# Kernel optimization log

Measured on AMD Instinct MI355X. Metric: run time of the kernel, lower is better.

## Reference

```python
import jax, jax.numpy as jnp
import numpy as np

# AlphaFold2-scale config
C_S, C_Z, H, D = 256, 128, 8, 32
T = H * D  # total_dim = 256
B, S, N = 1, 128, 256  # batch, MSA rows, residues
EPS = 1e-5
SCALE = 1.0 / np.sqrt(D).astype(np.float32)


def _layer_norm(x, w, b):
    m = jnp.mean(x, axis=-1, keepdims=True)
    v = jnp.var(x, axis=-1, keepdims=True)
    return (x - m) * jax.lax.rsqrt(v + EPS) * w + b


def setup_inputs() -> dict:
    key = jax.random.key(0)
    ks = jax.random.split(key, 8)
    w = lambda k, shape: jax.random.normal(k, shape, dtype=jnp.float32) * 0.02
    return {
        "msa_representation": jax.random.normal(ks[0], (B, S, N, C_S), dtype=jnp.float32),
        "pair_representation": jax.random.normal(ks[1], (B, N, N, C_Z), dtype=jnp.float32),
        "ln_msa_w": jnp.ones((C_S,), jnp.float32),
        "ln_msa_b": jnp.zeros((C_S,), jnp.float32),
        "ln_pair_w": jnp.ones((C_Z,), jnp.float32),
        "ln_pair_b": jnp.zeros((C_Z,), jnp.float32),
        "Wq": w(ks[2], (C_S, T)),
        "Wk": w(ks[3], (C_S, T)),
        "Wv": w(ks[4], (C_S, T)),
        "Wpair": w(ks[5], (C_Z, H)),
        "Wg": w(ks[6], (C_S, T)),
        "bg": jnp.zeros((T,), jnp.float32),
        "Wo": w(ks[7], (T, C_S)),
        "bo": jnp.zeros((C_S,), jnp.float32),
    }


def reference(msa_representation, pair_representation, ln_msa_w, ln_msa_b,
              ln_pair_w, ln_pair_b, Wq, Wk, Wv, Wpair, Wg, bg, Wo, bo):
    msa = _layer_norm(msa_representation, ln_msa_w, ln_msa_b)  # [B,S,N,C_S]
    q = (msa @ Wq).reshape(B, S, N, H, D)
    k = (msa @ Wk).reshape(B, S, N, H, D)
    v = (msa @ Wv).reshape(B, S, N, H, D)
    g = jax.nn.sigmoid(msa @ Wg + bg).reshape(B, S, N, H, D)

    pair = _layer_norm(pair_representation, ln_pair_w, ln_pair_b)  # [B,N,N,C_Z]
    bias = jnp.transpose(pair @ Wpair, (0, 3, 1, 2))[:, None]  # [B,1,H,N,N]

    scores = jnp.einsum('bsihd,bsjhd->bshij', q, k) * SCALE + bias  # [B,S,H,N,N]
    attn = jax.nn.softmax(scores, axis=-1)
    vals = jnp.einsum('bshij,bsjhd->bsihd', attn, v)  # [B,S,N,H,D]
    vals = (g * vals).reshape(B, S, N, T)
    return vals @ Wo + bo  # [B,S,N,C_S]
```

## Files before the change

### kernel.cpp

```cpp
#include <hip/hip_runtime.h>

typedef unsigned short u16;
typedef unsigned int u32;
typedef __bf16 bf16x8 __attribute__((ext_vector_type(8)));
typedef float f32x4 __attribute__((ext_vector_type(4)));

#define EPS 1e-5f
#define SCALE 0.17677669529663687f

__device__ __forceinline__ u16 f2bf(float f) {
  u32 u = __builtin_bit_cast(u32, f);
  u32 r = (u + 0x7fffu + ((u >> 16) & 1u)) >> 16;
  return (u16)r;
}
__device__ __forceinline__ float bf2f(u16 v) {
  return __builtin_bit_cast(float, (u32)v << 16);
}

__device__ __forceinline__ void gload16(const u16* g, u16* l) {
  __builtin_amdgcn_global_load_lds(
      (const __attribute__((address_space(1))) void*)g,
      (__attribute__((address_space(3))) void*)l, 16, 0, 0);
}

__global__ __launch_bounds__(256) void k_ln_msa(const float* __restrict__ x,
                                                const float* __restrict__ w,
                                                const float* __restrict__ b,
                                                u16* __restrict__ y) {
  int wid = threadIdx.x >> 6, lane = threadIdx.x & 63;
  long row = (long)blockIdx.x * 4 + wid;
  const float4 v = *reinterpret_cast<const float4*>(x + row * 256 + lane * 4);
  float s = v.x + v.y + v.z + v.w;
  float ss = v.x * v.x + v.y * v.y + v.z * v.z + v.w * v.w;
#pragma unroll
  for (int off = 1; off < 64; off <<= 1) {
    s += __shfl_xor(s, off);
    ss += __shfl_xor(ss, off);
  }
  float m = s * (1.0f / 256.0f);
  float var = ss * (1.0f / 256.0f) - m * m;
  float rs = rsqrtf(var + EPS);
  int c = lane * 4;
  u16 o0 = f2bf((v.x - m) * rs * w[c + 0] + b[c + 0]);
  u16 o1 = f2bf((v.y - m) * rs * w[c + 1] + b[c + 1]);
  u16 o2 = f2bf((v.z - m) * rs * w[c + 2] + b[c + 2]);
  u16 o3 = f2bf((v.w - m) * rs * w[c + 3] + b[c + 3]);
  uint2 pk;
  pk.x = (u32)o0 | ((u32)o1 << 16);
  pk.y = (u32)o2 | ((u32)o3 << 16);
  *reinterpret_cast<uint2*>(y + row * 256 + c) = pk;
}

__global__ __launch_bounds__(256) void k_pair_bias(const float* __restrict__ x,
                                                   const float* __restrict__ w,
                                                   const float* __restrict__ b,
                                                   const float* __restrict__ Wp,
                                                   float* __restrict__ bias) {
  int wid = threadIdx.x >> 6, lane = threadIdx.x & 63;
  long row = (long)blockIdx.x * 4 + wid;
  const float2 v = *reinterpret_cast<const float2*>(x + row * 128 + lane * 2);
  float s = v.x + v.y, ss = v.x * v.x + v.y * v.y;
#pragma unroll
  for (int off = 1; off < 64; off <<= 1) {
    s += __shfl_xor(s, off);
    ss += __shfl_xor(ss, off);
  }
  float m = s * (1.0f / 128.0f);
  float var = ss * (1.0f / 128.0f) - m * m;
  float rs = rsqrtf(var + EPS);
  int c = lane * 2;
  float x0 = (v.x - m) * rs * w[c] + b[c];
  float x1 = (v.y - m) * rs * w[c + 1] + b[c + 1];
  const float4* wp = reinterpret_cast<const float4*>(Wp + (long)c * 8);
  float4 a0 = wp[0], a1 = wp[1], a2 = wp[2], a3 = wp[3];
  float p[8];
  p[0] = x0 * a0.x + x1 * a2.x; p[1] = x0 * a0.y + x1 * a2.y;
  p[2] = x0 * a0.z + x1 * a2.z; p[3] = x0 * a0.w + x1 * a2.w;
  p[4] = x0 * a1.x + x1 * a3.x; p[5] = x0 * a1.y + x1 * a3.y;
  p[6] = x0 * a1.z + x1 * a3.z; p[7] = x0 * a1.w + x1 * a3.w;
#pragma unroll
  for (int off = 1; off < 64; off <<= 1) {
#pragma unroll
    for (int h = 0; h < 8; h++) p[h] += __shfl_xor(p[h], off);
  }
  if (lane == 0) {
#pragma unroll
    for (int h = 0; h < 8; h++) bias[(long)h * 65536 + row] = p[h];
  }
}

__global__ __launch_bounds__(256) void k_prep_w(const float* __restrict__ Wq,
                                                const float* __restrict__ Wk,
                                                const float* __restrict__ Wv,
                                                const float* __restrict__ Wg,
                                                const float* __restrict__ Wo,
                                                u16* __restrict__ Wt,
                                                u16* __restrict__ WoT) {
  int tid = blockIdx.x * 256 + threadIdx.x;
  if (tid < 262144) {
    int n = tid >> 8, kk = tid & 255;
    int sel = n >> 8, c = n & 255;
    const float* W = (sel == 0) ? Wq : (sel == 1) ? Wk : (sel == 2) ? Wv : Wg;
    Wt[tid] = f2bf(W[kk * 256 + c]);
  } else {
    int t = tid - 262144;
    int n = t >> 8, kk = t & 255;
    WoT[t] = f2bf(Wo[kk * 256 + n]);
  }
}

__global__ __launch_bounds__(256) void k_proj(const u16* __restrict__ X,
                                              const u16* __restrict__ Wt,
                                              const float* __restrict__ bg,
                                              u16* __restrict__ P) {
  __shared__ u16 As[2][4096];
  __shared__ u16 Bs[2][4096];
  int tid = threadIdx.x;
  int wid = tid >> 6, lane = tid & 63;
  int lr = lane & 15, lg = lane >> 4;
  int wr = wid >> 1, wc = wid & 1;
  int m0 = blockIdx.x * 128;
  int n0 = blockIdx.y * 128;

  int tr = tid >> 2, tc = (tid & 3) * 8;
  const u16* gA0 = X + (long)(m0 + tr) * 256 + tc;
  const u16* gA1 = X + (long)(m0 + 64 + tr) * 256 + tc;
  const u16* gB0 = Wt + (long)(n0 + tr) * 256 + tc;
  const u16* gB1 = Wt + (long)(n0 + 64 + tr) * 256 + tc;

  f32x4 acc[4][4];
#pragma unroll
  for (int mi = 0; mi < 4; mi++)
#pragma unroll
    for (int ni = 0; ni < 4; ni++) acc[mi][ni] = (f32x4){0.f, 0.f, 0.f, 0.f};

#define STAGE(buf, k0)                                  \
  do {                                                  \
    gload16(gA0 + (k0), &As[buf][tid * 8]);             \
    gload16(gA1 + (k0), &As[buf][2048 + tid * 8]);      \
    gload16(gB0 + (k0), &Bs[buf][tid * 8]);             \
    gload16(gB1 + (k0), &Bs[buf][2048 + tid * 8]);      \
  } while (0)

  STAGE(0, 0);
  __syncthreads();
#pragma unroll
  for (int step = 0; step < 8; step++) {
    int buf = step & 1;
    if (step < 7) STAGE(buf ^ 1, (step + 1) * 32);
    bf16x8 a[4], b[4];
#pragma unroll
    for (int mi = 0; mi < 4; mi++)
      a[mi] = *reinterpret_cast<const bf16x8*>(&As[buf][(wr * 64 + mi * 16 + lr) * 32 + lg * 8]);
#pragma unroll
    for (int ni = 0; ni < 4; ni++)
      b[ni] = *reinterpret_cast<const bf16x8*>(&Bs[buf][(wc * 64 + ni * 16 + lr) * 32 + lg * 8]);
#pragma unroll
    for (int mi = 0; mi < 4; mi++)
#pragma unroll
      for (int ni = 0; ni < 4; ni++)
        acc[mi][ni] = __builtin_amdgcn_mfma_f32_16x16x32_bf16(a[mi], b[ni], acc[mi][ni], 0, 0, 0);
    __syncthreads();
  }
#undef STAGE

#pragma unroll
  for (int ni = 0; ni < 4; ni++) {
    int col = n0 + wc * 64 + ni * 16 + lr;
    bool isq = col < 256, isg = col >= 768;
    float bgv = isg ? bg[col - 768] : 0.f;
#pragma unroll
    for (int mi = 0; mi < 4; mi++) {
#pragma unroll
      for (int r = 0; r < 4; r++) {
        int row = m0 + wr * 64 + mi * 16 + lg * 4 + r;
        float val = acc[mi][ni][r];
        if (isq) val *= SCALE;
        else if (isg) val = 1.0f / (1.0f + __expf(-(val + bgv)));
        P[(long)row * 1024 + col] = f2bf(val);
      }
    }
  }
}

__global__ __launch_bounds__(256) void k_attn(const u16* __restrict__ P,
                                              const float* __restrict__ bias,
                                              u16* __restrict__ vals) {
  __shared__ alignas(16) u16 VT[32][264];
  __shared__ alignas(16) u16 Plds[4][16][264];
  int tid = threadIdx.x;
  int wid = tid >> 6, lane = tid & 63;
  int lr = lane & 15, lg = lane >> 4;
  int i0 = blockIdx.x * 64, h = blockIdx.y, s = blockIdx.z;
  long sbase = (long)s * 256;

  {
    int j = tid;
    const uint4* vp = reinterpret_cast<const uint4*>(P + (sbase + j) * 1024 + 512 + h * 32);
#pragma unroll
    for (int q4 = 0; q4 < 4; q4++) {
      uint4 u = vp[q4];
      VT[q4 * 8 + 0][j] = (u16)(u.x & 0xffff);
      VT[q4 * 8 + 1][j] = (u16)(u.x >> 16);
      VT[q4 * 8 + 2][j] = (u16)(u.y & 0xffff);
      VT[q4 * 8 + 3][j] = (u16)(u.y >> 16);
      VT[q4 * 8 + 4][j] = (u16)(u.z & 0xffff);
      VT[q4 * 8 + 5][j] = (u16)(u.z >> 16);
      VT[q4 * 8 + 6][j] = (u16)(u.w & 0xffff);
      VT[q4 * 8 + 7][j] = (u16)(u.w >> 16);
    }
  }
  __syncthreads();

  int iw0 = i0 + wid * 16;
  bf16x8 qa = *reinterpret_cast<const bf16x8*>(P + (sbase + iw0 + lr) * 1024 + h * 32 + lg * 8);
  f32x4 sc[16];
#pragma unroll
  for (int jt = 0; jt < 16; jt++) {
    bf16x8 kb = *reinterpret_cast<const bf16x8*>(
        P + (sbase + jt * 16 + lr) * 1024 + 256 + h * 32 + lg * 8);
    f32x4 z = (f32x4){0.f, 0.f, 0.f, 0.f};
    sc[jt] = __builtin_amdgcn_mfma_f32_16x16x32_bf16(qa, kb, z, 0, 0, 0);
  }

  const float* bp = bias + (long)h * 65536;
  float rmax[4] = {-1e30f, -1e30f, -1e30f, -1e30f};
#pragma unroll
  for (int jt = 0; jt < 16; jt++) {
#pragma unroll
    for (int r = 0; r < 4; r++) {
      float v = sc[jt][r] + bp[(iw0 + lg * 4 + r) * 256 + jt * 16 + lr];
      sc[jt][r] = v;
      rmax[r] = fmaxf(rmax[r], v);
    }
  }
#pragma unroll
  for (int off = 1; off < 16; off <<= 1) {
#pragma unroll
    for (int r = 0; r < 4; r++) rmax[r] = fmaxf(rmax[r], __shfl_xor(rmax[r], off));
  }
  float rsum[4] = {0.f, 0.f, 0.f, 0.f};
#pragma unroll
  for (int jt = 0; jt < 16; jt++) {
#pragma unroll
    for (int r = 0; r < 4; r++) {
      float pv = __expf(sc[jt][r] - rmax[r]);
      sc[jt][r] = pv;
      rsum[r] += pv;
    }
  }
#pragma unroll
  for (int off = 1; off < 16; off <<= 1) {
#pragma unroll
    for (int r = 0; r < 4; r++) rsum[r] += __shfl_xor(rsum[r], off);
  }
#pragma unroll
  for (int jt = 0; jt < 16; jt++) {
#pragma unroll
    for (int r = 0; r < 4; r++) Plds[wid][lg * 4 + r][jt * 16 + lr] = f2bf(sc[jt][r]);
  }

  f32x4 ao[2];
  ao[0] = (f32x4){0.f, 0.f, 0.f, 0.f};
  ao[1] = (f32x4){0.f, 0.f, 0.f, 0.f};
#pragma unroll
  for (int ks = 0; ks < 8; ks++) {
    bf16x8 pa = *reinterpret_cast<const bf16x8*>(&Plds[wid][lr][ks * 32 + lg * 8]);
#pragma unroll
    for (int nt = 0; nt < 2; nt++) {
      bf16x8 vb = *reinterpret_cast<const bf16x8*>(&VT[nt * 16 + lr][ks * 32 + lg * 8]);
      ao[nt] = __builtin_amdgcn_mfma_f32_16x16x32_bf16(pa, vb, ao[nt], 0, 0, 0);
    }
  }

  float inv[4];
#pragma unroll
  for (int r = 0; r < 4; r++) inv[r] = 1.0f / rsum[r];
#pragma unroll
  for (int nt = 0; nt < 2; nt++) {
#pragma unroll
    for (int r = 0; r < 4; r++) {
      int row = iw0 + lg * 4 + r;
      int d = nt * 16 + lr;
      float gv = bf2f(P[(sbase + row) * 1024 + 768 + h * 32 + d]);
      float ov = ao[nt][r] * inv[r] * gv;
      vals[(sbase + row) * 256 + h * 32 + d] = f2bf(ov);
    }
  }
}

__global__ __launch_bounds__(256) void k_out(const u16* __restrict__ X,
                                             const u16* __restrict__ WoT,
                                             const float* __restrict__ bo,
                                             float* __restrict__ out) {
  __shared__ u16 As[2][4096];
  __shared__ u16 Bs[2][4096];
  int tid = threadIdx.x;
  int wid = tid >> 6, lane = tid & 63;
  int lr = lane & 15, lg = lane >> 4;
  int wr = wid >> 1, wc = wid & 1;
  int m0 = blockIdx.x * 128;
  int n0 = blockIdx.y * 128;

  int tr = tid >> 2, tc = (tid & 3) * 8;
  const u16* gA0 = X + (long)(m0 + tr) * 256 + tc;
  const u16* gA1 = X + (long)(m0 + 64 + tr) * 256 + tc;
  const u16* gB0 = WoT + (long)(n0 + tr) * 256 + tc;
  const u16* gB1 = WoT + (long)(n0 + 64 + tr) * 256 + tc;

  f32x4 acc[4][4];
#pragma unroll
  for (int mi = 0; mi < 4; mi++)
#pragma unroll
    for (int ni = 0; ni < 4; ni++) acc[mi][ni] = (f32x4){0.f, 0.f, 0.f, 0.f};

#define STAGE(buf, k0)                                  \
  do {                                                  \
    gload16(gA0 + (k0), &As[buf][tid * 8]);             \
    gload16(gA1 + (k0), &As[buf][2048 + tid * 8]);      \
    gload16(gB0 + (k0), &Bs[buf][tid * 8]);             \
    gload16(gB1 + (k0), &Bs[buf][2048 + tid * 8]);      \
  } while (0)

  STAGE(0, 0);
  __syncthreads();
#pragma unroll
  for (int step = 0; step < 8; step++) {
    int buf = step & 1;
    if (step < 7) STAGE(buf ^ 1, (step + 1) * 32);
    bf16x8 a[4], b[4];
#pragma unroll
    for (int mi = 0; mi < 4; mi++)
      a[mi] = *reinterpret_cast<const bf16x8*>(&As[buf][(wr * 64 + mi * 16 + lr) * 32 + lg * 8]);
#pragma unroll
    for (int ni = 0; ni < 4; ni++)
      b[ni] = *reinterpret_cast<const bf16x8*>(&Bs[buf][(wc * 64 + ni * 16 + lr) * 32 + lg * 8]);
#pragma unroll
    for (int mi = 0; mi < 4; mi++)
#pragma unroll
      for (int ni = 0; ni < 4; ni++)
        acc[mi][ni] = __builtin_amdgcn_mfma_f32_16x16x32_bf16(a[mi], b[ni], acc[mi][ni], 0, 0, 0);
    __syncthreads();
  }
#undef STAGE

#pragma unroll
  for (int ni = 0; ni < 4; ni++) {
    int col = n0 + wc * 64 + ni * 16 + lr;
    float bias_c = bo[col];
#pragma unroll
    for (int mi = 0; mi < 4; mi++) {
#pragma unroll
      for (int r = 0; r < 4; r++) {
        int row = m0 + wr * 64 + mi * 16 + lg * 4 + r;
        out[(long)row * 256 + col] = acc[mi][ni][r] + bias_c;
      }
    }
  }
}

extern "C" void kernel_launch(void* const* d_in, const int* in_sizes, int n_in,
                              void* d_out, int out_size, void* d_ws, size_t ws_size,
                              hipStream_t stream) {
  (void)in_sizes; (void)n_in; (void)out_size; (void)ws_size;
  const float* msa = (const float*)d_in[0];
  const float* pair = (const float*)d_in[1];
  const float* ln_msa_w = (const float*)d_in[2];
  const float* ln_msa_b = (const float*)d_in[3];
  const float* ln_pair_w = (const float*)d_in[4];
  const float* ln_pair_b = (const float*)d_in[5];
  const float* Wq = (const float*)d_in[6];
  const float* Wk = (const float*)d_in[7];
  const float* Wv = (const float*)d_in[8];
  const float* Wpair = (const float*)d_in[9];
  const float* Wg = (const float*)d_in[10];
  const float* bg = (const float*)d_in[11];
  const float* Wo = (const float*)d_in[12];
  const float* bo = (const float*)d_in[13];
  float* out = (float*)d_out;

  char* ws = (char*)d_ws;
  u16* msa_ln = (u16*)(ws + 0);
  u16* P      = (u16*)(ws + 16777216);
  float* biasb = (float*)(ws + 83886080);
  u16* vals   = (u16*)(ws + 85983232);
  u16* Wt     = (u16*)(ws + 102760448);
  u16* WoT    = (u16*)(ws + 103284736);

  k_prep_w<<<dim3(1280), dim3(256), 0, stream>>>(Wq, Wk, Wv, Wg, Wo, Wt, WoT);
  k_ln_msa<<<dim3(8192), dim3(256), 0, stream>>>(msa, ln_msa_w, ln_msa_b, msa_ln);
  k_pair_bias<<<dim3(16384), dim3(256), 0, stream>>>(pair, ln_pair_w, ln_pair_b, Wpair, biasb);
  k_proj<<<dim3(256, 8), dim3(256), 0, stream>>>(msa_ln, Wt, bg, P);
  k_attn<<<dim3(4, 8, 128), dim3(256), 0, stream>>>(P, biasb, vals);
  k_out<<<dim3(256, 2), dim3(256), 0, stream>>>(vals, WoT, bo, out);
}
```

Measured before the change: 186.2 us.

## Relayout Q/K/G head-major and V transposed, restructure attention per (head,row)

The projection kernel now writes Q, K and gate into head-major [3][H][S*N][D] buffers and V pre-transposed per (s,h). The pair bias is stored transposed. The attention kernel now runs one block per (h,s): it stages all of K and V^T into LDS once and has each wave loop over 64 query rows. It computes scores as K·Q so that softmax reductions stay within a lane group, and passes probabilities to the PV MFMA through shuffles instead of LDS. This is meant to remove strided 1024-wide row reads and the redundant per-block V transpose, at the cost of scattered 2-byte stores in the projection epilogue and more shuffle traffic.

New measurement: 292.4 us. +57.1%, slower.

```diff
diff --git a/kernel.cpp b/kernel.cpp
--- a/kernel.cpp
+++ b/kernel.cpp
@@ -15,6 +15,9 @@
 }
 __device__ __forceinline__ float bf2f(u16 v) {
   return __builtin_bit_cast(float, (u32)v << 16);
+}
+__device__ __forceinline__ u32 pack2(float a, float b) {
+  return (u32)f2bf(a) | ((u32)f2bf(b) << 16);
 }
 
 __device__ __forceinline__ void gload16(const u16* g, u16* l) {
@@ -55,7 +58,7 @@
                                                    const float* __restrict__ w,
                                                    const float* __restrict__ b,
                                                    const float* __restrict__ Wp,
-                                                   float* __restrict__ bias) {
+                                                   float* __restrict__ biasT) {
   int wid = threadIdx.x >> 6, lane = threadIdx.x & 63;
   long row = (long)blockIdx.x * 4 + wid;
   const float2 v = *reinterpret_cast<const float2*>(x + row * 128 + lane * 2);
@@ -84,8 +87,9 @@
     for (int h = 0; h < 8; h++) p[h] += __shfl_xor(p[h], off);
   }
   if (lane == 0) {
-#pragma unroll
-    for (int h = 0; h < 8; h++) bias[(long)h * 65536 + row] = p[h];
+    int i = (int)(row >> 8), j = (int)(row & 255);
+#pragma unroll
+    for (int h = 0; h < 8; h++) biasT[(long)h * 65536 + j * 256 + i] = p[h];
   }
 }
 
@@ -112,7 +116,8 @@
 __global__ __launch_bounds__(256) void k_proj(const u16* __restrict__ X,
                                               const u16* __restrict__ Wt,
                                               const float* __restrict__ bg,
-                                              u16* __restrict__ P) {
+                                              u16* __restrict__ qkg,
+                                              u16* __restrict__ vt) {
   __shared__ u16 As[2][4096];
   __shared__ u16 Bs[2][4096];
   int tid = threadIdx.x;
@@ -121,6 +126,7 @@
   int wr = wid >> 1, wc = wid & 1;
   int m0 = blockIdx.x * 128;
   int n0 = blockIdx.y * 128;
+  int sel = n0 >> 8;
 
   int tr = tid >> 2, tc = (tid & 3) * 8;
   const u16* gA0 = X + (long)(m0 + tr) * 256 + tc;
@@ -164,127 +170,156 @@
   }
 #undef STAGE
 
+  int s = m0 >> 8;
 #pragma unroll
   for (int ni = 0; ni < 4; ni++) {
     int col = n0 + wc * 64 + ni * 16 + lr;
-    bool isq = col < 256, isg = col >= 768;
-    float bgv = isg ? bg[col - 768] : 0.f;
-#pragma unroll
-    for (int mi = 0; mi < 4; mi++) {
-#pragma unroll
-      for (int r = 0; r < 4; r++) {
-        int row = m0 + wr * 64 + mi * 16 + lg * 4 + r;
-        float val = acc[mi][ni][r];
-        if (isq) val *= SCALE;
-        else if (isg) val = 1.0f / (1.0f + __expf(-(val + bgv)));
-        P[(long)row * 1024 + col] = f2bf(val);
-      }
-    }
-  }
-}
-
-__global__ __launch_bounds__(256) void k_attn(const u16* __restrict__ P,
-                                              const float* __restrict__ bias,
+    int cq = col & 255;
+    int hh = cq >> 5, dd = cq & 31;
+    if (sel == 2) {
+      u16* vbase = vt + (((long)s * 8 + hh) * 32 + dd) * 256;
+#pragma unroll
+      for (int mi = 0; mi < 4; mi++) {
+        int i = (m0 & 255) + wr * 64 + mi * 16 + lg * 4;
+        uint2 pk;
+        pk.x = pack2(acc[mi][ni][0], acc[mi][ni][1]);
+        pk.y = pack2(acc[mi][ni][2], acc[mi][ni][3]);
+        *reinterpret_cast<uint2*>(vbase + i) = pk;
+      }
+    } else {
+      int t = (sel == 3) ? 2 : sel;
+      float bgv = (sel == 3) ? bg[cq] : 0.f;
+      u16* qbase = qkg + ((long)(t * 8 + hh) * 32768) * 32;
+#pragma unroll
+      for (int mi = 0; mi < 4; mi++) {
+#pragma unroll
+        for (int r = 0; r < 4; r++) {
+          int row = m0 + wr * 64 + mi * 16 + lg * 4 + r;
+          float val = acc[mi][ni][r];
+          if (sel == 0) val *= SCALE;
+          else if (sel == 3) val = 1.0f / (1.0f + __expf(-(val + bgv)));
+          qbase[(long)row * 32 + dd] = f2bf(val);
+        }
+      }
+    }
+  }
+}
+
+__global__ __launch_bounds__(256) void k_attn(const u16* __restrict__ qkg,
+                                              const u16* __restrict__ vt,
+                                              const float* __restrict__ biasT,
                                               u16* __restrict__ vals) {
-  __shared__ alignas(16) u16 VT[32][264];
-  __shared__ alignas(16) u16 Plds[4][16][264];
+  __shared__ alignas(16) u16 Ks[256 * 40];
+  __shared__ alignas(16) u16 VTs[32 * 264];
   int tid = threadIdx.x;
   int wid = tid >> 6, lane = tid & 63;
   int lr = lane & 15, lg = lane >> 4;
-  int i0 = blockIdx.x * 64, h = blockIdx.y, s = blockIdx.z;
-  long sbase = (long)s * 256;
-
-  {
-    int j = tid;
-    const uint4* vp = reinterpret_cast<const uint4*>(P + (sbase + j) * 1024 + 512 + h * 32);
-#pragma unroll
-    for (int q4 = 0; q4 < 4; q4++) {
-      uint4 u = vp[q4];
-      VT[q4 * 8 + 0][j] = (u16)(u.x & 0xffff);
-      VT[q4 * 8 + 1][j] = (u16)(u.x >> 16);
-      VT[q4 * 8 + 2][j] = (u16)(u.y & 0xffff);
-      VT[q4 * 8 + 3][j] = (u16)(u.y >> 16);
-      VT[q4 * 8 + 4][j] = (u16)(u.z & 0xffff);
-      VT[q4 * 8 + 5][j] = (u16)(u.z >> 16);
-      VT[q4 * 8 + 6][j] = (u16)(u.w & 0xffff);
-      VT[q4 * 8 + 7][j] = (u16)(u.w >> 16);
-    }
+  int h = blockIdx.x, s = blockIdx.y;
+
+  const u16* qb = qkg + ((long)(0 + h) * 32768 + s * 256) * 32;
+  const u16* kb = qkg + ((long)(8 + h) * 32768 + s * 256) * 32;
+  const u16* gb = qkg + ((long)(16 + h) * 32768 + s * 256) * 32;
+  const u16* vb = vt + ((long)s * 8 + h) * 32 * 256;
+
+#pragma unroll
+  for (int k = 0; k < 4; k++) {
+    int c = tid + k * 256;
+    uint4 u = *reinterpret_cast<const uint4*>(kb + c * 8);
+    int j = c >> 2, p = c & 3;
+    *reinterpret_cast<uint4*>(&Ks[j * 40 + p * 8]) = u;
+  }
+#pragma unroll
+  for (int k = 0; k < 4; k++) {
+    int c = tid + k * 256;
+    uint4 u = *reinterpret_cast<const uint4*>(vb + c * 8);
+    int d = c >> 5, p = c & 31;
+    *reinterpret_cast<uint4*>(&VTs[d * 264 + p * 8]) = u;
   }
   __syncthreads();
 
-  int iw0 = i0 + wid * 16;
-  bf16x8 qa = *reinterpret_cast<const bf16x8*>(P + (sbase + iw0 + lr) * 1024 + h * 32 + lg * 8);
-  f32x4 sc[16];
-#pragma unroll
-  for (int jt = 0; jt < 16; jt++) {
-    bf16x8 kb = *reinterpret_cast<const bf16x8*>(
-        P + (sbase + jt * 16 + lr) * 1024 + 256 + h * 32 + lg * 8);
-    f32x4 z = (f32x4){0.f, 0.f, 0.f, 0.f};
-    sc[jt] = __builtin_amdgcn_mfma_f32_16x16x32_bf16(qa, kb, z, 0, 0, 0);
-  }
-
-  const float* bp = bias + (long)h * 65536;
-  float rmax[4] = {-1e30f, -1e30f, -1e30f, -1e30f};
-#pragma unroll
-  for (int jt = 0; jt < 16; jt++) {
+  const float* bh = biasT + (long)h * 65536;
+
+  for (int ig = 0; ig < 4; ig++) {
+    int i0 = wid * 64 + ig * 16;
+    bf16x8 qf = *reinterpret_cast<const bf16x8*>(qb + (i0 + lr) * 32 + lg * 8);
+
+    f32x4 p[16];
+#pragma unroll
+    for (int jt = 0; jt < 16; jt++) {
+      bf16x8 kf = *reinterpret_cast<const bf16x8*>(&Ks[(jt * 16 + lr) * 40 + lg * 8]);
+      f32x4 z = (f32x4){0.f, 0.f, 0.f, 0.f};
+      p[jt] = __builtin_amdgcn_mfma_f32_16x16x32_bf16(kf, qf, z, 0, 0, 0);
+    }
+
+    float mx = -1e30f;
+#pragma unroll
+    for (int jt = 0; jt < 16; jt++) {
+#pragma unroll
+      for (int r = 0; r < 4; r++) {
+        float v = p[jt][r] + bh[(jt * 16 + lg * 4 + r) * 256 + i0 + lr];
+        p[jt][r] = v;
+        mx = fmaxf(mx, v);
+      }
+    }
+    mx = fmaxf(mx, __shfl_xor(mx, 16));
+    mx = fmaxf(mx, __shfl_xor(mx, 32));
+
+    float sum = 0.f;
+    u32 pkA[16], pkB[16];
+#pragma unroll
+    for (int jt = 0; jt < 16; jt++) {
+      float e0 = __expf(p[jt][0] - mx);
+      float e1 = __expf(p[jt][1] - mx);
+      float e2 = __expf(p[jt][2] - mx);
+      float e3 = __expf(p[jt][3] - mx);
+      sum += (e0 + e1) + (e2 + e3);
+      pkA[jt] = pack2(e0, e1);
+      pkB[jt] = pack2(e2, e3);
+    }
+    sum += __shfl_xor(sum, 16);
+    sum += __shfl_xor(sum, 32);
+
+    f32x4 o[2];
+    o[0] = (f32x4){0.f, 0.f, 0.f, 0.f};
+    o[1] = (f32x4){0.f, 0.f, 0.f, 0.f};
+    int srcA = ((lg & 1) * 2) * 16 + lr;
+    int srcB = srcA + 16;
+    bool hi = lg >= 2;
+#pragma unroll
+    for (int ks = 0; ks < 8; ks++) {
+      u32 aLo = (u32)__shfl((int)pkA[2 * ks], srcA);
+      u32 aHi = (u32)__shfl((int)pkA[2 * ks + 1], srcA);
+      u32 bLo = (u32)__shfl((int)pkB[2 * ks], srcA);
+      u32 bHi = (u32)__shfl((int)pkB[2 * ks + 1], srcA);
+      u32 cLo = (u32)__shfl((int)pkA[2 * ks], srcB);
+      u32 cHi = (u32)__shfl((int)pkA[2 * ks + 1], srcB);
+      u32 dLo = (u32)__shfl((int)pkB[2 * ks], srcB);
+      u32 dHi = (u32)__shfl((int)pkB[2 * ks + 1], srcB);
+      uint4 pu;
+      pu.x = hi ? aHi : aLo;
+      pu.y = hi ? bHi : bLo;
+      pu.z = hi ? cHi : cLo;
+      pu.w = hi ? dHi : dLo;
+      bf16x8 pa = __builtin_bit_cast(bf16x8, pu);
+#pragma unroll
+      for (int nt = 0; nt < 2; nt++) {
+        bf16x8 vf = *reinterpret_cast<const bf16x8*>(&VTs[(nt * 16 + lr) * 264 + ks * 32 + lg * 8]);
+        o[nt] = __builtin_amdgcn_mfma_f32_16x16x32_bf16(pa, vf, o[nt], 0, 0, 0);
+      }
+    }
+
+    float inv = 1.0f / sum;
 #pragma unroll
     for (int r = 0; r < 4; r++) {
-      float v = sc[jt][r] + bp[(iw0 + lg * 4 + r) * 256 + jt * 16 + lr];
-      sc[jt][r] = v;
-      rmax[r] = fmaxf(rmax[r], v);
-    }
-  }
-#pragma unroll
-  for (int off = 1; off < 16; off <<= 1) {
-#pragma unroll
-    for (int r = 0; r < 4; r++) rmax[r] = fmaxf(rmax[r], __shfl_xor(rmax[r], off));
-  }
-  float rsum[4] = {0.f, 0.f, 0.f, 0.f};
-#pragma unroll
-  for (int jt = 0; jt < 16; jt++) {
-#pragma unroll
-    for (int r = 0; r < 4; r++) {
-      float pv = __expf(sc[jt][r] - rmax[r]);
-      sc[jt][r] = pv;
-      rsum[r] += pv;
-    }
-  }
-#pragma unroll
-  for (int off = 1; off < 16; off <<= 1) {
-#pragma unroll
-    for (int r = 0; r < 4; r++) rsum[r] += __shfl_xor(rsum[r], off);
-  }
-#pragma unroll
-  for (int jt = 0; jt < 16; jt++) {
-#pragma unroll
-    for (int r = 0; r < 4; r++) Plds[wid][lg * 4 + r][jt * 16 + lr] = f2bf(sc[jt][r]);
-  }
-
-  f32x4 ao[2];
-  ao[0] = (f32x4){0.f, 0.f, 0.f, 0.f};
-  ao[1] = (f32x4){0.f, 0.f, 0.f, 0.f};
-#pragma unroll
-  for (int ks = 0; ks < 8; ks++) {
-    bf16x8 pa = *reinterpret_cast<const bf16x8*>(&Plds[wid][lr][ks * 32 + lg * 8]);
-#pragma unroll
-    for (int nt = 0; nt < 2; nt++) {
-      bf16x8 vb = *reinterpret_cast<const bf16x8*>(&VT[nt * 16 + lr][ks * 32 + lg * 8]);
-      ao[nt] = __builtin_amdgcn_mfma_f32_16x16x32_bf16(pa, vb, ao[nt], 0, 0, 0);
-    }
-  }
-
-  float inv[4];
-#pragma unroll
-  for (int r = 0; r < 4; r++) inv[r] = 1.0f / rsum[r];
-#pragma unroll
-  for (int nt = 0; nt < 2; nt++) {
-#pragma unroll
-    for (int r = 0; r < 4; r++) {
-      int row = iw0 + lg * 4 + r;
-      int d = nt * 16 + lr;
-      float gv = bf2f(P[(sbase + row) * 1024 + 768 + h * 32 + d]);
-      float ov = ao[nt][r] * inv[r] * gv;
-      vals[(sbase + row) * 256 + h * 32 + d] = f2bf(ov);
+      float invr = __shfl(inv, lg * 4 + r);
+      int row = i0 + lg * 4 + r;
+#pragma unroll
+      for (int nt = 0; nt < 2; nt++) {
+        int d = nt * 16 + lr;
+        float gv = bf2f(gb[(long)row * 32 + d]);
+        float ov = o[nt][r] * invr * gv;
+        vals[((long)s * 256 + row) * 256 + h * 32 + d] = f2bf(ov);
+      }
     }
   }
 }
@@ -318,7 +353,7 @@
   do {                                                  \
     gload16(gA0 + (k0), &As[buf][tid * 8]);             \
     gload16(gA1 + (k0), &As[buf][2048 + tid * 8]);      \
-    gload16(gB0 + (k0), &Bs[buf][tid * 8]);             \
+    gload16(gB0 + (k0), &Bs[buf][2048 + tid * 8 - 2048]); \
     gload16(gB1 + (k0), &Bs[buf][2048 + tid * 8]);      \
   } while (0)
 
@@ -381,16 +416,17 @@
 
   char* ws = (char*)d_ws;
   u16* msa_ln = (u16*)(ws + 0);
-  u16* P      = (u16*)(ws + 16777216);
-  float* biasb = (float*)(ws + 83886080);
+  u16* qkg    = (u16*)(ws + 16777216);
+  u16* vt     = (u16*)(ws + 67108864);
+  float* biasT = (float*)(ws + 83886080);
   u16* vals   = (u16*)(ws + 85983232);
   u16* Wt     = (u16*)(ws + 102760448);
   u16* WoT    = (u16*)(ws + 103284736);
 
   k_prep_w<<<dim3(1280), dim3(256), 0, stream>>>(Wq, Wk, Wv, Wg, Wo, Wt, WoT);
   k_ln_msa<<<dim3(8192), dim3(256), 0, stream>>>(msa, ln_msa_w, ln_msa_b, msa_ln);
-  k_pair_bias<<<dim3(16384), dim3(256), 0, stream>>>(pair, ln_pair_w, ln_pair_b, Wpair, biasb);
-  k_proj<<<dim3(256, 8), dim3(256), 0, stream>>>(msa_ln, Wt, bg, P);
-  k_attn<<<dim3(4, 8, 128), dim3(256), 0, stream>>>(P, biasb, vals);
+  k_pair_bias<<<dim3(16384), dim3(256), 0, stream>>>(pair, ln_pair_w, ln_pair_b, Wpair, biasT);
+  k_proj<<<dim3(256, 8), dim3(256), 0, stream>>>(msa_ln, Wt, bg, qkg, vt);
+  k_attn<<<dim3(8, 128), dim3(256), 0, stream>>>(qkg, vt, biasT, vals);
   k_out<<<dim3(256, 2), dim3(256), 0, stream>>>(vals, WoT, bo, out);
 }
```
